# Kernel tuning notes

Hardware: AMD Instinct MI355X
Metric: run time of the kernel (lower is better)

## Reference

```python
import jax, jax.numpy as jnp
import numpy as np

T, K, D_SLOTS, D_IN, D_HID, EPSILON = 3, 11, 64, 128, 256, 1e-8


def _layer_norm(x, g, b, eps=1e-5):
    m = jnp.mean(x, axis=-1, keepdims=True)
    v = jnp.mean((x - m) ** 2, axis=-1, keepdims=True)
    return (x - m) * jax.lax.rsqrt(v + eps) * g + b


def _gru_cell(x, h, w_ih, w_hh, b_ih, b_hh):
    # torch.nn.GRUCell math; w_ih/w_hh stored as [D, 3D] (input-major)
    gx = x @ w_ih + b_ih
    gh = h @ w_hh + b_hh
    xr, xz, xn = jnp.split(gx, 3, axis=-1)
    hr, hz, hn = jnp.split(gh, 3, axis=-1)
    r = jax.nn.sigmoid(xr + hr)
    z = jax.nn.sigmoid(xz + hz)
    n = jnp.tanh(xn + r * hn)
    return (1.0 - z) * n + z * h


def setup_inputs() -> dict:
    key = jax.random.key(0)
    ks = jax.random.split(key, 12)
    B, N = 64, 4096
    s = 0.02
    return {
        "inputs": jax.random.normal(ks[0], (B, N, D_IN), jnp.float32),
        "ln_in_g": jnp.ones((D_IN,), jnp.float32),
        "ln_in_b": jnp.zeros((D_IN,), jnp.float32),
        "Wk": jax.random.normal(ks[1], (D_IN, D_SLOTS), jnp.float32) * s,
        "Wv": jax.random.normal(ks[2], (D_IN, D_SLOTS), jnp.float32) * s,
        "init_latents": jax.random.normal(ks[3], (1, K, D_SLOTS), jnp.float32),
        "ln_q_g": jnp.ones((D_SLOTS,), jnp.float32),
        "ln_q_b": jnp.zeros((D_SLOTS,), jnp.float32),
        "Wq": jax.random.normal(ks[4], (D_SLOTS, D_SLOTS), jnp.float32) * s,
        "w_ih": jax.random.normal(ks[5], (D_SLOTS, 3 * D_SLOTS), jnp.float32) * s,
        "w_hh": jax.random.normal(ks[6], (D_SLOTS, 3 * D_SLOTS), jnp.float32) * s,
        "b_ih": jnp.zeros((3 * D_SLOTS,), jnp.float32),
        "b_hh": jnp.zeros((3 * D_SLOTS,), jnp.float32),
        "ln_f_g": jnp.ones((D_SLOTS,), jnp.float32),
        "ln_f_b": jnp.zeros((D_SLOTS,), jnp.float32),
        "W1": jax.random.normal(ks[7], (D_SLOTS, D_HID), jnp.float32) * s,
        "b1": jnp.zeros((D_HID,), jnp.float32),
        "W2": jax.random.normal(ks[8], (D_HID, D_SLOTS), jnp.float32) * s,
        "b2": jnp.zeros((D_SLOTS,), jnp.float32),
    }


def reference(inputs, ln_in_g, ln_in_b, Wk, Wv, init_latents, ln_q_g, ln_q_b, Wq,
              w_ih, w_hh, b_ih, b_hh, ln_f_g, ln_f_b, W1, b1, W2, b2):
    B = inputs.shape[0]
    x = _layer_norm(inputs, ln_in_g, ln_in_b)          # [B,N,128]
    keys = x @ Wk                                       # [B,N,D]
    vals = x @ Wv                                       # [B,N,D]
    slots = jnp.broadcast_to(init_latents, (B, K, D_SLOTS))
    scale = D_SLOTS ** (-0.5)
    attn2 = None
    for _ in range(T):
        slots_prev = slots
        q = _layer_norm(slots, ln_q_g, ln_q_b) @ Wq     # [B,K,D]
        logits = scale * jnp.einsum('bnc,bmc->bnm', keys, q)  # [B,N,K]
        attn = jax.nn.softmax(logits, axis=-1) + EPSILON
        attn2 = attn
        attn_n = attn / jnp.sum(attn, axis=1, keepdims=True)   # competing norm over inputs
        updates = jnp.einsum('bnm,bnc->bmc', attn_n, vals)     # [B,K,D]
        slots = _gru_cell(updates.reshape(B * K, D_SLOTS),
                          slots_prev.reshape(B * K, D_SLOTS),
                          w_ih, w_hh, b_ih, b_hh).reshape(B, K, D_SLOTS)
        h = jax.nn.relu(_layer_norm(slots, ln_f_g, ln_f_b) @ W1 + b1)
        slots = slots + (h @ W2 + b2)
    return slots, attn2
```

## Files before the change

### kernel.cpp

```cpp
#include <hip/hip_runtime.h>

#define DIN   128
#define DSL   64
#define KSL   11
#define NTOK  4096
#define NB    64
#define NSPLIT 32
#define LN_EPS   1e-5f
#define ATTN_EPS 1e-8f
#define SCALE    0.125f

typedef __bf16 bf16x8 __attribute__((ext_vector_type(8)));
typedef float  f32x4  __attribute__((ext_vector_type(4)));

__global__ void k_prep(const float* __restrict__ Wk, const float* __restrict__ Wv,
                       const float* __restrict__ g, const float* __restrict__ b,
                       __bf16* __restrict__ WTf, float* __restrict__ EP) {
  if (blockIdx.x == 8) {
    const int c = threadIdx.x;
    if (c < 128) {
      const float* __restrict__ W = (c < 64) ? Wk : Wv;
      const int cc = c & 63;
      float G = 0.f, Bt = 0.f;
      for (int k = 0; k < 128; ++k) {
        const float w = W[k * 64 + cc];
        G += g[k] * w; Bt += b[k] * w;
      }
      EP[c] = G; EP[128 + c] = Bt;
    }
    return;
  }
  const int t = blockIdx.x * 256 + threadIdx.x;
  const int fid = t >> 6, lane = t & 63;
  const int ks = fid >> 3, nt = fid & 7;
  const int col = nt * 16 + (lane & 15);
  const int kb  = ks * 32 + (lane >> 4) * 8;
  union { uint4 u; __bf16 h[8]; } o;
#pragma unroll
  for (int j = 0; j < 8; ++j) {
    const int k = kb + j;
    const float v = ((col < 64) ? Wk[k * 64 + col] : Wv[k * 64 + (col - 64)]) * g[k];
    o.h[j] = (__bf16)v;
  }
  *((uint4*)WTf + t) = o.u;
}

__launch_bounds__(256)
__global__ void k_lnproj(const float* __restrict__ inp, const __bf16* __restrict__ WTf,
                         const float* __restrict__ EP, __bf16* __restrict__ keys,
                         __bf16* __restrict__ valsT) {
  __shared__ __bf16 Xs[4][16][136];
  __shared__ float rowstats[4][16][2];
  const int tid = threadIdx.x, wave = tid >> 6, lane = tid & 63;
  const int half = lane >> 5, hl = lane & 31;
  const int t = lane & 15, g = lane >> 4;
  const bf16x8* __restrict__ Wv8 = (const bf16x8*)WTf;

  float4 cur[8], nxt[8];
  {
    const int r0 = blockIdx.x * 256 + wave * 16;
#pragma unroll
    for (int p = 0; p < 8; ++p)
      cur[p] = *(const float4*)(inp + (size_t)(r0 + 2 * p + half) * DIN + hl * 4);
  }

  for (int it = 0; it < 4; ++it) {
    const int rbase = blockIdx.x * 256 + it * 64 + wave * 16;
    if (it < 3) {
      const int rn = rbase + 64;
#pragma unroll
      for (int p = 0; p < 8; ++p)
        nxt[p] = *(const float4*)(inp + (size_t)(rn + 2 * p + half) * DIN + hl * 4);
    }
    float s[8], sq[8];
#pragma unroll
    for (int p = 0; p < 8; ++p) {
      s[p]  = cur[p].x + cur[p].y + cur[p].z + cur[p].w;
      sq[p] = cur[p].x * cur[p].x + cur[p].y * cur[p].y
            + cur[p].z * cur[p].z + cur[p].w * cur[p].w;
      union { ushort4 u; __bf16 h[4]; } pk;
      pk.h[0] = (__bf16)cur[p].x; pk.h[1] = (__bf16)cur[p].y;
      pk.h[2] = (__bf16)cur[p].z; pk.h[3] = (__bf16)cur[p].w;
      *(ushort4*)&Xs[wave][2 * p + half][hl * 4] = pk.u;
    }
#pragma unroll
    for (int o = 16; o > 0; o >>= 1) {
#pragma unroll
      for (int p = 0; p < 8; ++p) { s[p] += __shfl_xor(s[p], o); sq[p] += __shfl_xor(sq[p], o); }
    }
    if (hl < 8) {
      const int p = hl;
      const float m = s[p] * (1.f / 128.f);
      const float rstd = rsqrtf(sq[p] * (1.f / 128.f) - m * m + LN_EPS);
      rowstats[wave][2 * p + half][0] = m;
      rowstats[wave][2 * p + half][1] = rstd;
    }
    f32x4 acc[8] = {};
#pragma unroll
    for (int ks = 0; ks < 4; ++ks) {
      const bf16x8 xf = *(const bf16x8*)&Xs[wave][t][ks * 32 + g * 8];
#pragma unroll
      for (int nt = 0; nt < 8; ++nt) {
        const bf16x8 wf = Wv8[(ks * 8 + nt) * 64 + lane];
        acc[nt] = __builtin_amdgcn_mfma_f32_16x16x32_bf16(wf, xf, acc[nt], 0, 0, 0);
      }
    }
    const float2 mrs = *(const float2*)&rowstats[wave][t][0];
    const float rstd = mrs.y, mm = mrs.x * mrs.y;
    const int bidx = rbase >> 12;
    const int tIB  = (rbase & 4095) + t;
#pragma unroll
    for (int nt = 0; nt < 8; ++nt) {
      const float4 Gv = *(const float4*)(EP + nt * 16 + g * 4);
      const float4 Bv = *(const float4*)(EP + 128 + nt * 16 + g * 4);
      const float o0 = rstd * acc[nt][0] - mm * Gv.x + Bv.x;
      const float o1 = rstd * acc[nt][1] - mm * Gv.y + Bv.y;
      const float o2 = rstd * acc[nt][2] - mm * Gv.z + Bv.z;
      const float o3 = rstd * acc[nt][3] - mm * Gv.w + Bv.w;
      if (nt < 4) {
        union { unsigned long long u; __bf16 h[4]; } pk;
        pk.h[0] = (__bf16)o0; pk.h[1] = (__bf16)o1; pk.h[2] = (__bf16)o2; pk.h[3] = (__bf16)o3;
        *(unsigned long long*)&keys[(size_t)(rbase + t) * 64 + nt * 16 + g * 4] = pk.u;
      } else {
        const int vc = (nt - 4) * 16 + g * 4;
        valsT[((size_t)bidx * 64 + vc + 0) * NTOK + tIB] = (__bf16)o0;
        valsT[((size_t)bidx * 64 + vc + 1) * NTOK + tIB] = (__bf16)o1;
        valsT[((size_t)bidx * 64 + vc + 2) * NTOK + tIB] = (__bf16)o2;
        valsT[((size_t)bidx * 64 + vc + 3) * NTOK + tIB] = (__bf16)o3;
      }
    }
#pragma unroll
    for (int p = 0; p < 8; ++p) cur[p] = nxt[p];
  }
}

__global__ void k_init(const float* __restrict__ init_lat, const float* __restrict__ qg,
                       const float* __restrict__ qb, const float* __restrict__ Wq,
                       float* __restrict__ slots, float* __restrict__ q) {
  const int b = blockIdx.x;
  const int k = threadIdx.x >> 6, c = threadIdx.x & 63;
  const float s = init_lat[k * DSL + c];
  slots[(size_t)(b * KSL + k) * DSL + c] = s;
  float sum = s, sq = s * s;
#pragma unroll
  for (int o = 32; o > 0; o >>= 1) { sum += __shfl_xor(sum, o); sq += __shfl_xor(sq, o); }
  const float m = sum * (1.f / 64.f);
  const float rstd = rsqrtf(sq * (1.f / 64.f) - m * m + LN_EPS);
  const float qn = (s - m) * rstd * qg[c] + qb[c];
  float acc = 0.f;
  for (int i = 0; i < DSL; ++i) acc += __shfl(qn, i) * Wq[i * DSL + c];
  q[(size_t)(b * KSL + k) * DSL + c] = acc * SCALE;
}

__launch_bounds__(64)
__global__ void k_attn(const __bf16* __restrict__ keys, const __bf16* __restrict__ valsT,
                       const float* __restrict__ q, float* __restrict__ Upart,
                       float* __restrict__ Spart, float* __restrict__ attn_out) {
  __shared__ __bf16 P[2][16][72];
  const int b = blockIdx.x >> 5, sp = blockIdx.x & 31;
  const int lane = threadIdx.x;
  const int g = lane >> 4, t = lane & 15;

  bf16x8 qf[2];
#pragma unroll
  for (int ks = 0; ks < 2; ++ks) {
    float4 q0 = {0.f, 0.f, 0.f, 0.f}, q1 = {0.f, 0.f, 0.f, 0.f};
    if (t < KSL) {
      const float* __restrict__ qp = q + (size_t)(b * KSL + t) * DSL + ks * 32 + g * 8;
      q0 = *(const float4*)qp; q1 = *(const float4*)(qp + 4);
    }
    qf[ks][0] = (__bf16)q0.x; qf[ks][1] = (__bf16)q0.y;
    qf[ks][2] = (__bf16)q0.z; qf[ks][3] = (__bf16)q0.w;
    qf[ks][4] = (__bf16)q1.x; qf[ks][5] = (__bf16)q1.y;
    qf[ks][6] = (__bf16)q1.z; qf[ks][7] = (__bf16)q1.w;
  }

  const __bf16* __restrict__ kbase = keys + ((size_t)b * NTOK + sp * 128) * DSL;
  float sacc[4] = {0.f, 0.f, 0.f, 0.f};
  f32x4 U[4] = {};

#pragma unroll
  for (int gr = 0; gr < 2; ++gr) {
    const int tb = gr * 64;
#pragma unroll
    for (int tile = 0; tile < 4; ++tile) {
      f32x4 c = {};
#pragma unroll
      for (int ks = 0; ks < 2; ++ks) {
        const bf16x8 kf = *(const bf16x8*)(kbase + (size_t)(tb + tile * 16 + t) * DSL
                                           + ks * 32 + g * 8);
        c = __builtin_amdgcn_mfma_f32_16x16x32_bf16(qf[ks], kf, c, 0, 0, 0);
      }
      float lg[4];
#pragma unroll
      for (int r = 0; r < 4; ++r)
        lg[r] = (4 * g + r < KSL) ? c[r] : -1e30f;
      float mx = fmaxf(fmaxf(lg[0], lg[1]), fmaxf(lg[2], lg[3]));
      mx = fmaxf(mx, __shfl_xor(mx, 16));
      mx = fmaxf(mx, __shfl_xor(mx, 32));
      float e[4];
#pragma unroll
      for (int r = 0; r < 4; ++r) e[r] = __expf(lg[r] - mx);
      float se = e[0] + e[1] + e[2] + e[3];
      se += __shfl_xor(se, 16);
      se += __shfl_xor(se, 32);
      const float inv = 1.f / se;
#pragma unroll
      for (int r = 0; r < 4; ++r) {
        const float a = e[r] * inv + ATTN_EPS;
        sacc[r] += a;
        P[gr][4 * g + r][tile * 16 + t] = (__bf16)a;
        if (attn_out && 4 * g + r < KSL)
          attn_out[((size_t)b * NTOK + sp * 128 + tb + tile * 16 + t) * KSL + 4 * g + r] = a;
      }
    }
#pragma unroll
    for (int ks = 0; ks < 2; ++ks) {
      const bf16x8 pf = *(const bf16x8*)&P[gr][t][ks * 32 + g * 8];
#pragma unroll
      for (int ct = 0; ct < 4; ++ct) {
        const bf16x8 vf = *(const bf16x8*)(valsT + ((size_t)b * DSL + ct * 16 + t) * NTOK
                                           + sp * 128 + tb + ks * 32 + g * 8);
        U[ct] = __builtin_amdgcn_mfma_f32_16x16x32_bf16(pf, vf, U[ct], 0, 0, 0);
      }
    }
  }

  float* __restrict__ up = Upart + (size_t)(b * NSPLIT + sp) * (KSL * DSL);
#pragma unroll
  for (int ct = 0; ct < 4; ++ct)
#pragma unroll
    for (int r = 0; r < 4; ++r)
      if (4 * g + r < KSL) up[(4 * g + r) * DSL + ct * 16 + t] = U[ct][r];

#pragma unroll
  for (int r = 0; r < 4; ++r) {
#pragma unroll
    for (int o = 1; o < 16; o <<= 1) sacc[r] += __shfl_xor(sacc[r], o);
  }
  if (t == 0) {
    float* __restrict__ spp = Spart + (size_t)(b * NSPLIT + sp) * 16;
#pragma unroll
    for (int r = 0; r < 4; ++r) spp[4 * g + r] = sacc[r];
  }
}

__launch_bounds__(64)
__global__ void k_update(const float* __restrict__ Upart, const float* __restrict__ Spart,
                         float* __restrict__ slots, const float* __restrict__ w_ih,
                         const float* __restrict__ w_hh, const float* __restrict__ b_ih,
                         const float* __restrict__ b_hh, const float* __restrict__ fg,
                         const float* __restrict__ fb, const float* __restrict__ W1,
                         const float* __restrict__ b1v, const float* __restrict__ W2,
                         const float* __restrict__ b2v, const float* __restrict__ qg,
                         const float* __restrict__ qbv, const float* __restrict__ Wq,
                         float* __restrict__ q, float* __restrict__ out_slots) {
  const int row = blockIdx.x;
  const int c = threadIdx.x;
  const int b = row / 11, k = row - b * 11;

  float u = 0.f;
  for (int s = 0; s < NSPLIT; ++s)
    u += Upart[((size_t)(b * NSPLIT + s) * KSL + k) * DSL + c];
  float ss = 0.f;
  for (int s = 0; s < NSPLIT; ++s)
    ss += Spart[(size_t)(b * NSPLIT + s) * 16 + k];
  u /= ss;

  const float h = slots[(size_t)row * DSL + c];

  float gr = b_ih[c], gz = b_ih[64 + c], gn = b_ih[128 + c];
  float hr = b_hh[c], hz = b_hh[64 + c], hn = b_hh[128 + c];
  for (int i = 0; i < 64; ++i) {
    const float ui = __shfl(u, i), hi = __shfl(h, i);
    gr += ui * w_ih[i * 192 + c];       hr += hi * w_hh[i * 192 + c];
    gz += ui * w_ih[i * 192 + 64 + c];  hz += hi * w_hh[i * 192 + 64 + c];
    gn += ui * w_ih[i * 192 + 128 + c]; hn += hi * w_hh[i * 192 + 128 + c];
  }
  const float r = 1.f / (1.f + __expf(-(gr + hr)));
  const float z = 1.f / (1.f + __expf(-(gz + hz)));
  const float nn = tanhf(gn + r * hn);
  float sv = (1.f - z) * nn + z * h;

  float sum = sv, sq = sv * sv;
#pragma unroll
  for (int o = 32; o > 0; o >>= 1) { sum += __shfl_xor(sum, o); sq += __shfl_xor(sq, o); }
  float m = sum * (1.f / 64.f);
  float rstd = rsqrtf(sq * (1.f / 64.f) - m * m + LN_EPS);
  const float sl = (sv - m) * rstd * fg[c] + fb[c];

  float h0 = b1v[c], h1 = b1v[64 + c], h2 = b1v[128 + c], h3 = b1v[192 + c];
  for (int i = 0; i < 64; ++i) {
    const float si = __shfl(sl, i);
    h0 += si * W1[i * 256 + c];        h1 += si * W1[i * 256 + 64 + c];
    h2 += si * W1[i * 256 + 128 + c];  h3 += si * W1[i * 256 + 192 + c];
  }
  h0 = fmaxf(h0, 0.f); h1 = fmaxf(h1, 0.f); h2 = fmaxf(h2, 0.f); h3 = fmaxf(h3, 0.f);

  float o = b2v[c];
  for (int j = 0; j < 64; ++j) o += __shfl(h0, j) * W2[j * DSL + c];
  for (int j = 0; j < 64; ++j) o += __shfl(h1, j) * W2[(64 + j) * DSL + c];
  for (int j = 0; j < 64; ++j) o += __shfl(h2, j) * W2[(128 + j) * DSL + c];
  for (int j = 0; j < 64; ++j) o += __shfl(h3, j) * W2[(192 + j) * DSL + c];
  sv += o;

  slots[(size_t)row * DSL + c] = sv;
  if (out_slots) out_slots[(size_t)row * DSL + c] = sv;

  float s2 = sv, q2 = sv * sv;
#pragma unroll
  for (int o2 = 32; o2 > 0; o2 >>= 1) { s2 += __shfl_xor(s2, o2); q2 += __shfl_xor(q2, o2); }
  m = s2 * (1.f / 64.f);
  rstd = rsqrtf(q2 * (1.f / 64.f) - m * m + LN_EPS);
  const float qn = (sv - m) * rstd * qg[c] + qbv[c];
  float qa = 0.f;
  for (int i = 0; i < 64; ++i) qa += __shfl(qn, i) * Wq[i * DSL + c];
  q[(size_t)row * DSL + c] = qa * SCALE;
}

extern "C" void kernel_launch(void* const* d_in, const int* in_sizes, int n_in,
                              void* d_out, int out_size, void* d_ws, size_t ws_size,
                              hipStream_t stream) {
  const float* inp  = (const float*)d_in[0];
  const float* lng  = (const float*)d_in[1];
  const float* lnb  = (const float*)d_in[2];
  const float* Wk   = (const float*)d_in[3];
  const float* Wv   = (const float*)d_in[4];
  const float* init = (const float*)d_in[5];
  const float* qg   = (const float*)d_in[6];
  const float* qbb  = (const float*)d_in[7];
  const float* Wq   = (const float*)d_in[8];
  const float* wih  = (const float*)d_in[9];
  const float* whh  = (const float*)d_in[10];
  const float* bih  = (const float*)d_in[11];
  const float* bhh  = (const float*)d_in[12];
  const float* fg   = (const float*)d_in[13];
  const float* fb   = (const float*)d_in[14];
  const float* W1   = (const float*)d_in[15];
  const float* b1   = (const float*)d_in[16];
  const float* W2   = (const float*)d_in[17];
  const float* b2   = (const float*)d_in[18];

  char* wsb = (char*)d_ws;
  __bf16* keys  = (__bf16*)wsb;
  __bf16* valsT = keys + (size_t)NB * NTOK * DSL;
  __bf16* WTf   = valsT + (size_t)NB * DSL * NTOK;
  float*  EP    = (float*)(WTf + 16384);
  float* slots = EP + 256;
  float* q     = slots + NB * KSL * DSL;
  float* Upart = q + NB * KSL * DSL;
  float* Spart = Upart + (size_t)NB * NSPLIT * KSL * DSL;

  float* out_slots = (float*)d_out;
  float* out_attn  = (float*)d_out + NB * KSL * DSL;

  k_prep<<<9, 256, 0, stream>>>(Wk, Wv, lng, lnb, WTf, EP);
  k_lnproj<<<1024, 256, 0, stream>>>(inp, WTf, EP, keys, valsT);
  k_init<<<NB, KSL * 64, 0, stream>>>(init, qg, qbb, Wq, slots, q);
  for (int t = 0; t < 3; ++t) {
    k_attn<<<NB * NSPLIT, 64, 0, stream>>>(keys, valsT, q, Upart, Spart,
                                           t == 2 ? out_attn : nullptr);
    k_update<<<NB * KSL, 64, 0, stream>>>(Upart, Spart, slots, wih, whh, bih, bhh,
                                          fg, fb, W1, b1, W2, b2, qg, qbb, Wq, q,
                                          t == 2 ? out_slots : nullptr);
  }
}
```

Before: 190.9 us.

## Shrink lnproj blocks, batch attn loads/softmax, split update across two waves

k_lnproj now processes 64 rows per block over 4096 blocks, replacing the 4-iteration software-pipelined loop with one pass. k_attn loads all key and value fragments for a 64-token group up front and batches the four tiles' QK MFMAs and softmax reductions, which increases memory-level and instruction-level parallelism. k_update uses two waves that each handle half the reduction ranges and combine partial sums through shared memory, shortening the serial matvec chains at the cost of extra barriers.

```diff
diff --git a/kernel.cpp b/kernel.cpp
--- a/kernel.cpp
+++ b/kernel.cpp
@@ -54,83 +54,69 @@
   const int tid = threadIdx.x, wave = tid >> 6, lane = tid & 63;
   const int half = lane >> 5, hl = lane & 31;
   const int t = lane & 15, g = lane >> 4;
+  const int rbase = blockIdx.x * 64 + wave * 16;
+
+  float4 xr[8];
+#pragma unroll
+  for (int p = 0; p < 8; ++p)
+    xr[p] = *(const float4*)(inp + (size_t)(rbase + 2 * p + half) * DIN + hl * 4);
+
+  float s[8], sq[8];
+#pragma unroll
+  for (int p = 0; p < 8; ++p) {
+    s[p]  = xr[p].x + xr[p].y + xr[p].z + xr[p].w;
+    sq[p] = xr[p].x * xr[p].x + xr[p].y * xr[p].y + xr[p].z * xr[p].z + xr[p].w * xr[p].w;
+    union { ushort4 u; __bf16 h[4]; } pk;
+    pk.h[0] = (__bf16)xr[p].x; pk.h[1] = (__bf16)xr[p].y;
+    pk.h[2] = (__bf16)xr[p].z; pk.h[3] = (__bf16)xr[p].w;
+    *(ushort4*)&Xs[wave][2 * p + half][hl * 4] = pk.u;
+  }
+#pragma unroll
+  for (int o = 16; o > 0; o >>= 1) {
+#pragma unroll
+    for (int p = 0; p < 8; ++p) { s[p] += __shfl_xor(s[p], o); sq[p] += __shfl_xor(sq[p], o); }
+  }
+  if (hl < 8) {
+    const int p = hl;
+    const float m = s[p] * (1.f / 128.f);
+    const float rstd = rsqrtf(sq[p] * (1.f / 128.f) - m * m + LN_EPS);
+    rowstats[wave][2 * p + half][0] = m;
+    rowstats[wave][2 * p + half][1] = rstd;
+  }
   const bf16x8* __restrict__ Wv8 = (const bf16x8*)WTf;
-
-  float4 cur[8], nxt[8];
-  {
-    const int r0 = blockIdx.x * 256 + wave * 16;
-#pragma unroll
-    for (int p = 0; p < 8; ++p)
-      cur[p] = *(const float4*)(inp + (size_t)(r0 + 2 * p + half) * DIN + hl * 4);
-  }
-
-  for (int it = 0; it < 4; ++it) {
-    const int rbase = blockIdx.x * 256 + it * 64 + wave * 16;
-    if (it < 3) {
-      const int rn = rbase + 64;
-#pragma unroll
-      for (int p = 0; p < 8; ++p)
-        nxt[p] = *(const float4*)(inp + (size_t)(rn + 2 * p + half) * DIN + hl * 4);
-    }
-    float s[8], sq[8];
-#pragma unroll
-    for (int p = 0; p < 8; ++p) {
-      s[p]  = cur[p].x + cur[p].y + cur[p].z + cur[p].w;
-      sq[p] = cur[p].x * cur[p].x + cur[p].y * cur[p].y
-            + cur[p].z * cur[p].z + cur[p].w * cur[p].w;
-      union { ushort4 u; __bf16 h[4]; } pk;
-      pk.h[0] = (__bf16)cur[p].x; pk.h[1] = (__bf16)cur[p].y;
-      pk.h[2] = (__bf16)cur[p].z; pk.h[3] = (__bf16)cur[p].w;
-      *(ushort4*)&Xs[wave][2 * p + half][hl * 4] = pk.u;
-    }
-#pragma unroll
-    for (int o = 16; o > 0; o >>= 1) {
-#pragma unroll
-      for (int p = 0; p < 8; ++p) { s[p] += __shfl_xor(s[p], o); sq[p] += __shfl_xor(sq[p], o); }
-    }
-    if (hl < 8) {
-      const int p = hl;
-      const float m = s[p] * (1.f / 128.f);
-      const float rstd = rsqrtf(sq[p] * (1.f / 128.f) - m * m + LN_EPS);
-      rowstats[wave][2 * p + half][0] = m;
-      rowstats[wave][2 * p + half][1] = rstd;
-    }
-    f32x4 acc[8] = {};
-#pragma unroll
-    for (int ks = 0; ks < 4; ++ks) {
-      const bf16x8 xf = *(const bf16x8*)&Xs[wave][t][ks * 32 + g * 8];
-#pragma unroll
-      for (int nt = 0; nt < 8; ++nt) {
-        const bf16x8 wf = Wv8[(ks * 8 + nt) * 64 + lane];
-        acc[nt] = __builtin_amdgcn_mfma_f32_16x16x32_bf16(wf, xf, acc[nt], 0, 0, 0);
-      }
-    }
-    const float2 mrs = *(const float2*)&rowstats[wave][t][0];
-    const float rstd = mrs.y, mm = mrs.x * mrs.y;
-    const int bidx = rbase >> 12;
-    const int tIB  = (rbase & 4095) + t;
+  f32x4 acc[8] = {};
+#pragma unroll
+  for (int ks = 0; ks < 4; ++ks) {
+    const bf16x8 xf = *(const bf16x8*)&Xs[wave][t][ks * 32 + g * 8];
 #pragma unroll
     for (int nt = 0; nt < 8; ++nt) {
-      const float4 Gv = *(const float4*)(EP + nt * 16 + g * 4);
-      const float4 Bv = *(const float4*)(EP + 128 + nt * 16 + g * 4);
-      const float o0 = rstd * acc[nt][0] - mm * Gv.x + Bv.x;
-      const float o1 = rstd * acc[nt][1] - mm * Gv.y + Bv.y;
-      const float o2 = rstd * acc[nt][2] - mm * Gv.z + Bv.z;
-      const float o3 = rstd * acc[nt][3] - mm * Gv.w + Bv.w;
-      if (nt < 4) {
-        union { unsigned long long u; __bf16 h[4]; } pk;
-        pk.h[0] = (__bf16)o0; pk.h[1] = (__bf16)o1; pk.h[2] = (__bf16)o2; pk.h[3] = (__bf16)o3;
-        *(unsigned long long*)&keys[(size_t)(rbase + t) * 64 + nt * 16 + g * 4] = pk.u;
-      } else {
-        const int vc = (nt - 4) * 16 + g * 4;
-        valsT[((size_t)bidx * 64 + vc + 0) * NTOK + tIB] = (__bf16)o0;
-        valsT[((size_t)bidx * 64 + vc + 1) * NTOK + tIB] = (__bf16)o1;
-        valsT[((size_t)bidx * 64 + vc + 2) * NTOK + tIB] = (__bf16)o2;
-        valsT[((size_t)bidx * 64 + vc + 3) * NTOK + tIB] = (__bf16)o3;
-      }
-    }
-#pragma unroll
-    for (int p = 0; p < 8; ++p) cur[p] = nxt[p];
+      const bf16x8 wf = Wv8[(ks * 8 + nt) * 64 + lane];
+      acc[nt] = __builtin_amdgcn_mfma_f32_16x16x32_bf16(wf, xf, acc[nt], 0, 0, 0);
+    }
+  }
+  const float2 mrs = *(const float2*)&rowstats[wave][t][0];
+  const float rstd = mrs.y, mm = mrs.x * mrs.y;
+  const int bidx = rbase >> 12;
+  const int tIB  = (rbase & 4095) + t;
+#pragma unroll
+  for (int nt = 0; nt < 8; ++nt) {
+    const float4 Gv = *(const float4*)(EP + nt * 16 + g * 4);
+    const float4 Bv = *(const float4*)(EP + 128 + nt * 16 + g * 4);
+    const float o0 = rstd * acc[nt][0] - mm * Gv.x + Bv.x;
+    const float o1 = rstd * acc[nt][1] - mm * Gv.y + Bv.y;
+    const float o2 = rstd * acc[nt][2] - mm * Gv.z + Bv.z;
+    const float o3 = rstd * acc[nt][3] - mm * Gv.w + Bv.w;
+    if (nt < 4) {
+      union { unsigned long long u; __bf16 h[4]; } pk;
+      pk.h[0] = (__bf16)o0; pk.h[1] = (__bf16)o1; pk.h[2] = (__bf16)o2; pk.h[3] = (__bf16)o3;
+      *(unsigned long long*)&keys[(size_t)(rbase + t) * 64 + nt * 16 + g * 4] = pk.u;
+    } else {
+      const int vc = (nt - 4) * 16 + g * 4;
+      valsT[((size_t)bidx * 64 + vc + 0) * NTOK + tIB] = (__bf16)o0;
+      valsT[((size_t)bidx * 64 + vc + 1) * NTOK + tIB] = (__bf16)o1;
+      valsT[((size_t)bidx * 64 + vc + 2) * NTOK + tIB] = (__bf16)o2;
+      valsT[((size_t)bidx * 64 + vc + 3) * NTOK + tIB] = (__bf16)o3;
+    }
   }
 }
 
@@ -176,38 +162,62 @@
   }
 
   const __bf16* __restrict__ kbase = keys + ((size_t)b * NTOK + sp * 128) * DSL;
+  const __bf16* __restrict__ vbase = valsT + (size_t)b * DSL * NTOK + sp * 128;
   float sacc[4] = {0.f, 0.f, 0.f, 0.f};
   f32x4 U[4] = {};
 
 #pragma unroll
   for (int gr = 0; gr < 2; ++gr) {
     const int tb = gr * 64;
+    bf16x8 kf[4][2];
+#pragma unroll
+    for (int tile = 0; tile < 4; ++tile)
+#pragma unroll
+      for (int ks = 0; ks < 2; ++ks)
+        kf[tile][ks] = *(const bf16x8*)(kbase + (size_t)(tb + tile * 16 + t) * DSL
+                                        + ks * 32 + g * 8);
+    bf16x8 vf[2][4];
+#pragma unroll
+    for (int ks = 0; ks < 2; ++ks)
+#pragma unroll
+      for (int ct = 0; ct < 4; ++ct)
+        vf[ks][ct] = *(const bf16x8*)(vbase + (size_t)(ct * 16 + t) * NTOK
+                                      + tb + ks * 32 + g * 8);
+    f32x4 c[4] = {};
+#pragma unroll
+    for (int ks = 0; ks < 2; ++ks)
+#pragma unroll
+      for (int tile = 0; tile < 4; ++tile)
+        c[tile] = __builtin_amdgcn_mfma_f32_16x16x32_bf16(qf[ks], kf[tile][ks], c[tile], 0, 0, 0);
+    float lg[4][4], mx[4];
 #pragma unroll
     for (int tile = 0; tile < 4; ++tile) {
-      f32x4 c = {};
-#pragma unroll
-      for (int ks = 0; ks < 2; ++ks) {
-        const bf16x8 kf = *(const bf16x8*)(kbase + (size_t)(tb + tile * 16 + t) * DSL
-                                           + ks * 32 + g * 8);
-        c = __builtin_amdgcn_mfma_f32_16x16x32_bf16(qf[ks], kf, c, 0, 0, 0);
-      }
-      float lg[4];
 #pragma unroll
       for (int r = 0; r < 4; ++r)
-        lg[r] = (4 * g + r < KSL) ? c[r] : -1e30f;
-      float mx = fmaxf(fmaxf(lg[0], lg[1]), fmaxf(lg[2], lg[3]));
-      mx = fmaxf(mx, __shfl_xor(mx, 16));
-      mx = fmaxf(mx, __shfl_xor(mx, 32));
-      float e[4];
-#pragma unroll
-      for (int r = 0; r < 4; ++r) e[r] = __expf(lg[r] - mx);
-      float se = e[0] + e[1] + e[2] + e[3];
-      se += __shfl_xor(se, 16);
-      se += __shfl_xor(se, 32);
-      const float inv = 1.f / se;
+        lg[tile][r] = (4 * g + r < KSL) ? c[tile][r] : -1e30f;
+      mx[tile] = fmaxf(fmaxf(lg[tile][0], lg[tile][1]), fmaxf(lg[tile][2], lg[tile][3]));
+    }
+#pragma unroll
+    for (int tile = 0; tile < 4; ++tile) mx[tile] = fmaxf(mx[tile], __shfl_xor(mx[tile], 16));
+#pragma unroll
+    for (int tile = 0; tile < 4; ++tile) mx[tile] = fmaxf(mx[tile], __shfl_xor(mx[tile], 32));
+    float se[4];
+#pragma unroll
+    for (int tile = 0; tile < 4; ++tile) {
+#pragma unroll
+      for (int r = 0; r < 4; ++r) lg[tile][r] = __expf(lg[tile][r] - mx[tile]);
+      se[tile] = lg[tile][0] + lg[tile][1] + lg[tile][2] + lg[tile][3];
+    }
+#pragma unroll
+    for (int tile = 0; tile < 4; ++tile) se[tile] += __shfl_xor(se[tile], 16);
+#pragma unroll
+    for (int tile = 0; tile < 4; ++tile) se[tile] += __shfl_xor(se[tile], 32);
+#pragma unroll
+    for (int tile = 0; tile < 4; ++tile) {
+      const float inv = 1.f / se[tile];
 #pragma unroll
       for (int r = 0; r < 4; ++r) {
-        const float a = e[r] * inv + ATTN_EPS;
+        const float a = lg[tile][r] * inv + ATTN_EPS;
         sacc[r] += a;
         P[gr][4 * g + r][tile * 16 + t] = (__bf16)a;
         if (attn_out && 4 * g + r < KSL)
@@ -218,11 +228,8 @@
     for (int ks = 0; ks < 2; ++ks) {
       const bf16x8 pf = *(const bf16x8*)&P[gr][t][ks * 32 + g * 8];
 #pragma unroll
-      for (int ct = 0; ct < 4; ++ct) {
-        const bf16x8 vf = *(const bf16x8*)(valsT + ((size_t)b * DSL + ct * 16 + t) * NTOK
-                                           + sp * 128 + tb + ks * 32 + g * 8);
-        U[ct] = __builtin_amdgcn_mfma_f32_16x16x32_bf16(pf, vf, U[ct], 0, 0, 0);
-      }
+      for (int ct = 0; ct < 4; ++ct)
+        U[ct] = __builtin_amdgcn_mfma_f32_16x16x32_bf16(pf, vf[ks][ct], U[ct], 0, 0, 0);
     }
   }
 
@@ -245,7 +252,7 @@
   }
 }
 
-__launch_bounds__(64)
+__launch_bounds__(128)
 __global__ void k_update(const float* __restrict__ Upart, const float* __restrict__ Spart,
                          float* __restrict__ slots, const float* __restrict__ w_ih,
                          const float* __restrict__ w_hh, const float* __restrict__ b_ih,
@@ -255,28 +262,43 @@
                          const float* __restrict__ b2v, const float* __restrict__ qg,
                          const float* __restrict__ qbv, const float* __restrict__ Wq,
                          float* __restrict__ q, float* __restrict__ out_slots) {
+  __shared__ float rU[2][64];
+  __shared__ float rS[2];
+  __shared__ float rG[2][6][64];
+  __shared__ float rH[2][4][64];
+  __shared__ float rO[2][64];
+  __shared__ float rQ[2][64];
+  const int w = threadIdx.x >> 6, c = threadIdx.x & 63;
   const int row = blockIdx.x;
-  const int c = threadIdx.x;
   const int b = row / 11, k = row - b * 11;
 
-  float u = 0.f;
-  for (int s = 0; s < NSPLIT; ++s)
-    u += Upart[((size_t)(b * NSPLIT + s) * KSL + k) * DSL + c];
-  float ss = 0.f;
-  for (int s = 0; s < NSPLIT; ++s)
-    ss += Spart[(size_t)(b * NSPLIT + s) * 16 + k];
-  u /= ss;
-
+  float upi = 0.f, ssp = 0.f;
+  for (int s = w * 16; s < w * 16 + 16; ++s) {
+    upi += Upart[((size_t)(b * NSPLIT + s) * KSL + k) * DSL + c];
+    ssp += Spart[(size_t)(b * NSPLIT + s) * 16 + k];
+  }
+  rU[w][c] = upi;
+  if (c == 0) rS[w] = ssp;
   const float h = slots[(size_t)row * DSL + c];
-
-  float gr = b_ih[c], gz = b_ih[64 + c], gn = b_ih[128 + c];
-  float hr = b_hh[c], hz = b_hh[64 + c], hn = b_hh[128 + c];
-  for (int i = 0; i < 64; ++i) {
+  __syncthreads();
+  const float u = (rU[0][c] + rU[1][c]) / (rS[0] + rS[1]);
+
+  float gr = 0.f, gz = 0.f, gn = 0.f, hr = 0.f, hz = 0.f, hn = 0.f;
+  for (int i = w * 32; i < w * 32 + 32; ++i) {
     const float ui = __shfl(u, i), hi = __shfl(h, i);
     gr += ui * w_ih[i * 192 + c];       hr += hi * w_hh[i * 192 + c];
     gz += ui * w_ih[i * 192 + 64 + c];  hz += hi * w_hh[i * 192 + 64 + c];
     gn += ui * w_ih[i * 192 + 128 + c]; hn += hi * w_hh[i * 192 + 128 + c];
   }
+  rG[w][0][c] = gr; rG[w][1][c] = gz; rG[w][2][c] = gn;
+  rG[w][3][c] = hr; rG[w][4][c] = hz; rG[w][5][c] = hn;
+  __syncthreads();
+  gr = rG[0][0][c] + rG[1][0][c] + b_ih[c];
+  gz = rG[0][1][c] + rG[1][1][c] + b_ih[64 + c];
+  gn = rG[0][2][c] + rG[1][2][c] + b_ih[128 + c];
+  hr = rG[0][3][c] + rG[1][3][c] + b_hh[c];
+  hz = rG[0][4][c] + rG[1][4][c] + b_hh[64 + c];
+  hn = rG[0][5][c] + rG[1][5][c] + b_hh[128 + c];
   const float r = 1.f / (1.f + __expf(-(gr + hr)));
   const float z = 1.f / (1.f + __expf(-(gz + hz)));
   const float nn = tanhf(gn + r * hn);
@@ -289,23 +311,30 @@
   float rstd = rsqrtf(sq * (1.f / 64.f) - m * m + LN_EPS);
   const float sl = (sv - m) * rstd * fg[c] + fb[c];
 
-  float h0 = b1v[c], h1 = b1v[64 + c], h2 = b1v[128 + c], h3 = b1v[192 + c];
-  for (int i = 0; i < 64; ++i) {
+  float h0 = 0.f, h1 = 0.f, h2 = 0.f, h3 = 0.f;
+  for (int i = w * 32; i < w * 32 + 32; ++i) {
     const float si = __shfl(sl, i);
     h0 += si * W1[i * 256 + c];        h1 += si * W1[i * 256 + 64 + c];
     h2 += si * W1[i * 256 + 128 + c];  h3 += si * W1[i * 256 + 192 + c];
   }
-  h0 = fmaxf(h0, 0.f); h1 = fmaxf(h1, 0.f); h2 = fmaxf(h2, 0.f); h3 = fmaxf(h3, 0.f);
-
-  float o = b2v[c];
-  for (int j = 0; j < 64; ++j) o += __shfl(h0, j) * W2[j * DSL + c];
-  for (int j = 0; j < 64; ++j) o += __shfl(h1, j) * W2[(64 + j) * DSL + c];
-  for (int j = 0; j < 64; ++j) o += __shfl(h2, j) * W2[(128 + j) * DSL + c];
-  for (int j = 0; j < 64; ++j) o += __shfl(h3, j) * W2[(192 + j) * DSL + c];
-  sv += o;
-
-  slots[(size_t)row * DSL + c] = sv;
-  if (out_slots) out_slots[(size_t)row * DSL + c] = sv;
+  rH[w][0][c] = h0; rH[w][1][c] = h1; rH[w][2][c] = h2; rH[w][3][c] = h3;
+  __syncthreads();
+  h0 = fmaxf(rH[0][0][c] + rH[1][0][c] + b1v[c], 0.f);
+  h1 = fmaxf(rH[0][1][c] + rH[1][1][c] + b1v[64 + c], 0.f);
+  h2 = fmaxf(rH[0][2][c] + rH[1][2][c] + b1v[128 + c], 0.f);
+  h3 = fmaxf(rH[0][3][c] + rH[1][3][c] + b1v[192 + c], 0.f);
+
+  float o = 0.f;
+  {
+    const float ha = (w == 0) ? h0 : h2;
+    const float hb = (w == 0) ? h1 : h3;
+    const int base = w * 128;
+    for (int j = 0; j < 64; ++j) o += __shfl(ha, j) * W2[(base + j) * DSL + c];
+    for (int j = 0; j < 64; ++j) o += __shfl(hb, j) * W2[(base + 64 + j) * DSL + c];
+  }
+  rO[w][c] = o;
+  __syncthreads();
+  sv += rO[0][c] + rO[1][c] + b2v[c];
 
   float s2 = sv, q2 = sv * sv;
 #pragma unroll
@@ -314,8 +343,14 @@
   rstd = rsqrtf(q2 * (1.f / 64.f) - m * m + LN_EPS);
   const float qn = (sv - m) * rstd * qg[c] + qbv[c];
   float qa = 0.f;
-  for (int i = 0; i < 64; ++i) qa += __shfl(qn, i) * Wq[i * DSL + c];
-  q[(size_t)row * DSL + c] = qa * SCALE;
+  for (int i = w * 32; i < w * 32 + 32; ++i) qa += __shfl(qn, i) * Wq[i * DSL + c];
+  rQ[w][c] = qa;
+  __syncthreads();
+  if (w == 0) {
+    slots[(size_t)row * DSL + c] = sv;
+    if (out_slots) out_slots[(size_t)row * DSL + c] = sv;
+    q[(size_t)row * DSL + c] = (rQ[0][c] + rQ[1][c]) * SCALE;
+  }
 }
 
 extern "C" void kernel_launch(void* const* d_in, const int* in_sizes, int n_in,
@@ -355,13 +390,13 @@
   float* out_attn  = (float*)d_out + NB * KSL * DSL;
 
   k_prep<<<9, 256, 0, stream>>>(Wk, Wv, lng, lnb, WTf, EP);
-  k_lnproj<<<1024, 256, 0, stream>>>(inp, WTf, EP, keys, valsT);
+  k_lnproj<<<4096, 256, 0, stream>>>(inp, WTf, EP, keys, valsT);
   k_init<<<NB, KSL * 64, 0, stream>>>(init, qg, qbb, Wq, slots, q);
   for (int t = 0; t < 3; ++t) {
     k_attn<<<NB * NSPLIT, 64, 0, stream>>>(keys, valsT, q, Upart, Spart,
                                            t == 2 ? out_attn : nullptr);
-    k_update<<<NB * KSL, 64, 0, stream>>>(Upart, Spart, slots, wih, whh, bih, bhh,
-                                          fg, fb, W1, b1, W2, b2, qg, qbb, Wq, q,
-                                          t == 2 ? out_slots : nullptr);
-  }
-}
+    k_update<<<NB * KSL, 128, 0, stream>>>(Upart, Spart, slots, wih, whh, bih, bhh,
+                                           fg, fb, W1, b1, W2, b2, qg, qbb, Wq, q,
+                                           t == 2 ? out_slots : nullptr);
+  }
+}
```

New measurement: 152.9 us. 19.9% less time.
